# Kernel tuning notes

Hardware: AMD Instinct MI355X
Metric: run time of the kernel (lower is better)

## Reference

```python
import jax, jax.numpy as jnp
import numpy as np

N_HEADS = 16
HEAD_DIM = 64
D_MODEL = N_HEADS * HEAD_DIM  # 1024


def setup_inputs() -> dict:
    key = jax.random.key(0)
    ks = jax.random.split(key, 6)
    B, S, D = 2, 2048, D_MODEL
    s = 0.02
    return {
        "hidden_states": jax.random.normal(ks[0], (B, S, D), jnp.float32),
        "position_bias": jax.random.normal(ks[1], (1, N_HEADS, S, S), jnp.float32),
        "Wq": jax.random.normal(ks[2], (D, D), jnp.float32) * s,
        "Wk": jax.random.normal(ks[3], (D, D), jnp.float32) * s,
        "Wv": jax.random.normal(ks[4], (D, D), jnp.float32) * s,
        "Wo": jax.random.normal(ks[5], (D, D), jnp.float32) * s,
    }


def reference(hidden_states, position_bias, Wq, Wk, Wv, Wo):
    B, S, D = hidden_states.shape

    def split_heads(x):  # [B,S,D] -> [B,H,S,hd]
        return x.reshape(B, S, N_HEADS, HEAD_DIM).transpose(0, 2, 1, 3)

    q = split_heads(hidden_states @ Wq)
    k = split_heads(hidden_states @ Wk)
    v = split_heads(hidden_states @ Wv)

    # T5 attention: NO 1/sqrt(d) scaling; additive relative-position bias.
    scores = jnp.einsum("bhqd,bhkd->bhqk", q, k) + position_bias
    attn = jax.nn.softmax(scores.astype(jnp.float32), axis=-1).astype(scores.dtype)
    ctx = jnp.einsum("bhqk,bhkd->bhqd", attn, v)
    ctx = ctx.transpose(0, 2, 1, 3).reshape(B, S, D)
    return ctx @ Wo
```

## Files before the change

kernel.cpp:

```cpp
#include <hip/hip_runtime.h>
#include <hip/hip_bf16.h>
#include <stdint.h>

typedef __bf16 bf16_t;
typedef __bf16 bf16x8 __attribute__((ext_vector_type(8)));
typedef float  f32x4  __attribute__((ext_vector_type(4)));

#define S_LEN 2048
#define NH    16
#define HD    64
#define DM    1024
#define BATCH 2
#define M_TOT (BATCH * S_LEN)
#define SM_SHIFT 18.0f

__device__ __forceinline__ void gload16(const void* g, void* l) {
    __builtin_amdgcn_global_load_lds(
        (const __attribute__((address_space(1))) unsigned int*)g,
        (__attribute__((address_space(3))) unsigned int*)l, 16, 0, 0);
}

__global__ void convert_h(const float* __restrict__ X, bf16_t* __restrict__ Y, int n) {
    int i = (blockIdx.x * 256 + threadIdx.x) * 4;
    if (i >= n) return;
    float4 v = *(const float4*)(X + i);
    union { bf16_t h[4]; uint2 u; } pk;
    pk.h[0] = (bf16_t)v.x; pk.h[1] = (bf16_t)v.y;
    pk.h[2] = (bf16_t)v.z; pk.h[3] = (bf16_t)v.w;
    *(uint2*)(Y + i) = pk.u;
}

__global__ void convert_transpose_w(const float* __restrict__ W, bf16_t* __restrict__ Wt) {
    __shared__ float tile[32][33];
    const int tid = threadIdx.x;
    const int tx = tid & 31, ty = tid >> 5;
    const int bx = blockIdx.x * 32, by = blockIdx.y * 32;
#pragma unroll
    for (int it = 0; it < 4; ++it)
        tile[ty + it * 8][tx] = W[(size_t)(by + ty + it * 8) * DM + bx + tx];
    __syncthreads();
#pragma unroll
    for (int it = 0; it < 4; ++it)
        Wt[(size_t)(bx + ty + it * 8) * DM + by + tx] = (bf16_t)tile[tx][ty + it * 8];
}

template<int BN, int EPI>
__global__ __launch_bounds__(256)
void gemm_glds(const bf16_t* __restrict__ A, const bf16_t* __restrict__ Bt,
               float* __restrict__ Cf, bf16_t* __restrict__ Qb, bf16_t* __restrict__ Kb,
               bf16_t* __restrict__ Vtb, int M, int N, int K)
{
    constexpr int WN = BN / 2;
    constexpr int NJ = WN / 16;
    constexpr int RB = BN / 32;
    __shared__ bf16_t smem[16640];
    bf16_t* At  = smem;
    bf16_t* Bts = smem + 8192;

    const int tid  = threadIdx.x;
    const int lane = tid & 63;
    const int wave = tid >> 6;
    const int lc = lane & 15;
    const int l4 = lane >> 4;
    const int wr = wave >> 1, wc = wave & 1;
    const int m0 = blockIdx.y * 128;
    const int n0 = blockIdx.x * BN;
    const int srow = tid >> 3;
    const int scol = (tid & 7) * 8;

    f32x4 acc[4][NJ] = {};

    for (int k0 = 0; k0 < K; k0 += 64) {
        __syncthreads();
#pragma unroll
        for (int ro = 0; ro < 4; ++ro)
            gload16(A + (size_t)(m0 + ro * 32 + srow) * K + k0 + scol,
                    At + ro * 2048 + wave * 512);
#pragma unroll
        for (int ro = 0; ro < RB; ++ro)
            gload16(Bt + (size_t)(n0 + ro * 32 + srow) * K + k0 + scol,
                    Bts + ro * 2048 + wave * 512);
        __syncthreads();

        bf16x8 af[2][4], bfr[2][NJ];
#pragma unroll
        for (int kk = 0; kk < 2; ++kk) {
#pragma unroll
            for (int i = 0; i < 4; ++i)
                af[kk][i] = *(const bf16x8*)(At + (wr * 64 + i * 16 + lc) * 64 + kk * 32 + l4 * 8);
#pragma unroll
            for (int j = 0; j < NJ; ++j)
                bfr[kk][j] = *(const bf16x8*)(Bts + (wc * WN + j * 16 + lc) * 64 + kk * 32 + l4 * 8);
        }
#pragma unroll
        for (int kk = 0; kk < 2; ++kk)
#pragma unroll
            for (int i = 0; i < 4; ++i)
#pragma unroll
                for (int j = 0; j < NJ; ++j)
                    acc[i][j] = __builtin_amdgcn_mfma_f32_16x16x32_bf16(af[kk][i], bfr[kk][j], acc[i][j], 0, 0, 0);
    }

    if (EPI == 1) {
#pragma unroll
        for (int i = 0; i < 4; ++i)
#pragma unroll
            for (int j = 0; j < NJ; ++j)
#pragma unroll
                for (int r = 0; r < 4; ++r) {
                    int m = m0 + wr * 64 + i * 16 + l4 * 4 + r;
                    int n = n0 + wc * WN + j * 16 + lc;
                    Cf[(size_t)m * N + n] = acc[i][j][r];
                }
    } else {
        const int sel = n0 >> 10;
        if (sel < 2) {
            bf16_t* Dst = sel == 0 ? Qb : Kb;
#pragma unroll
            for (int i = 0; i < 4; ++i)
#pragma unroll
                for (int j = 0; j < NJ; ++j)
#pragma unroll
                    for (int r = 0; r < 4; ++r) {
                        int m = m0 + wr * 64 + i * 16 + l4 * 4 + r;
                        int n = (n0 & 1023) + wc * WN + j * 16 + lc;
                        int b = m >> 11, s = m & 2047, h = n >> 6, d = n & 63;
                        Dst[(((size_t)(b * NH + h)) * S_LEN + s) * HD + d] = (bf16_t)acc[i][j][r];
                    }
        } else {
            __syncthreads();
            bf16_t* Ct = smem;
#pragma unroll
            for (int i = 0; i < 4; ++i)
#pragma unroll
                for (int j = 0; j < NJ; ++j)
#pragma unroll
                    for (int r = 0; r < 4; ++r) {
                        int ml = wr * 64 + i * 16 + l4 * 4 + r;
                        int nl = wc * WN + j * 16 + lc;
                        Ct[nl * 130 + ml] = (bf16_t)acc[i][j][r];
                    }
            __syncthreads();
            const int rr = tid >> 1, c0 = (tid & 1) * 64;
            const int nn = (n0 - 2048) + rr;
            const int hh = nn >> 6, dd = nn & 63;
            const int bb = m0 >> 11, s0 = m0 & 2047;
            bf16_t* dst = Vtb + (((size_t)(bb * NH + hh)) * HD + dd) * S_LEN + s0 + c0;
            const bf16_t* srcr = Ct + rr * 130 + c0;
#pragma unroll
            for (int u = 0; u < 8; ++u)
                *(uint4*)(dst + u * 8) = *(const uint4*)(srcr + u * 8);
        }
    }
}

__global__ __launch_bounds__(256, 1)
void attn_kernel(const bf16_t* __restrict__ Q, const bf16_t* __restrict__ Kin,
                 const bf16_t* __restrict__ Vt, const float* __restrict__ bias,
                 bf16_t* __restrict__ Ctx)
{
    const int tid  = threadIdx.x;
    const int lane = tid & 63;
    const int wave = tid >> 6;
    const int lc = lane & 15;
    const int l4 = lane >> 4;

    const int f   = blockIdx.x;
    const int xcd = f & 7;
    const int kk_ = f >> 3;
    const int h   = xcd * 2 + (kk_ >> 4);
    const int qt  = kk_ & 15;
    const int qw  = qt * 128 + wave * 32;

    __shared__ bf16_t Kt[2][2][64 * 64];
    __shared__ bf16_t Vs[2][2][64 * 64];
    __shared__ bf16_t Pt[4][2][32 * 72];

    const bf16_t* Qg[2]; const bf16_t* Kg[2]; const bf16_t* Vg[2];
#pragma unroll
    for (int b = 0; b < 2; ++b) {
        const int bh = b * NH + h;
        Qg[b] = Q   + (size_t)bh * S_LEN * HD;
        Kg[b] = Kin + (size_t)bh * S_LEN * HD;
        Vg[b] = Vt  + (size_t)bh * HD * S_LEN;
    }
    const float* Bg = bias + (size_t)h * S_LEN * S_LEN;

    bf16x8 qf[2][2][2];
#pragma unroll
    for (int b = 0; b < 2; ++b)
#pragma unroll
        for (int i = 0; i < 2; ++i)
#pragma unroll
            for (int kk = 0; kk < 2; ++kk)
                qf[b][i][kk] = *(const bf16x8*)(Qg[b] + (size_t)(qw + i * 16 + lc) * HD + kk * 32 + l4 * 8);

    f32x4 cacc[2][2][4] = {};
    float lsum[2][2][4] = {};

    const int r0   = lane >> 3;
    const int gsrc = (lane & 7) ^ r0;

    auto stage = [&](int t, int pbuf) {
        const int kv0 = t * 64;
#pragma unroll
        for (int c = 0; c < 2; ++c) {
            const int row = c * 32 + wave * 8 + r0;
            const int ldsoff = (c * 32 + wave * 8) * 64;
#pragma unroll
            for (int b = 0; b < 2; ++b) {
                gload16(Kg[b] + (size_t)(kv0 + row) * HD + gsrc * 8, &Kt[b][pbuf][ldsoff]);
                gload16(Vg[b] + (size_t)row * S_LEN + kv0 + gsrc * 8, &Vs[b][pbuf][ldsoff]);
            }
        }
    };

    auto loadbias = [&](int t, float (&bv)[2][4][4]) {
        const int kv0 = t * 64;
#pragma unroll
        for (int i = 0; i < 2; ++i)
#pragma unroll
            for (int r = 0; r < 4; ++r) {
                const float* bp = Bg + (size_t)(qw + i * 16 + l4 * 4 + r) * S_LEN + kv0 + lc;
#pragma unroll
                for (int j = 0; j < 4; ++j)
                    bv[i][j][r] = bp[j * 16] - SM_SHIFT;
            }
    };

    auto round = [&](int t, float (&bcur)[2][4][4], float (&bnext)[2][4][4]) {
        const int buf = t & 1;
        if (t < 31) {
            stage(t + 1, buf ^ 1);
            loadbias(t + 1, bnext);
        }
#pragma unroll
        for (int b = 0; b < 2; ++b) {
            f32x4 sa[2][4] = {};
#pragma unroll
            for (int kk = 0; kk < 2; ++kk) {
                bf16x8 kf[4];
#pragma unroll
                for (int j = 0; j < 4; ++j)
                    kf[j] = *(const bf16x8*)(&Kt[b][buf][(j * 16 + lc) * 64 + (((kk * 4 + l4) ^ (lc & 7)) * 8)]);
#pragma unroll
                for (int i = 0; i < 2; ++i)
#pragma unroll
                    for (int j = 0; j < 4; ++j)
                        sa[i][j] = __builtin_amdgcn_mfma_f32_16x16x32_bf16(qf[b][i][kk], kf[j], sa[i][j], 0, 0, 0);
            }
            bf16_t* Pw = Pt[wave][b];
#pragma unroll
            for (int i = 0; i < 2; ++i)
#pragma unroll
                for (int r = 0; r < 4; ++r) {
                    float p0 = __expf(sa[i][0][r] + bcur[i][0][r]);
                    float p1 = __expf(sa[i][1][r] + bcur[i][1][r]);
                    float p2 = __expf(sa[i][2][r] + bcur[i][2][r]);
                    float p3 = __expf(sa[i][3][r] + bcur[i][3][r]);
                    lsum[b][i][r] += (p0 + p1) + (p2 + p3);
                    const int rowo = (i * 16 + l4 * 4 + r) * 72 + lc;
                    Pw[rowo]      = (bf16_t)p0;
                    Pw[rowo + 16] = (bf16_t)p1;
                    Pw[rowo + 32] = (bf16_t)p2;
                    Pw[rowo + 48] = (bf16_t)p3;
                }
#pragma unroll
            for (int ks = 0; ks < 2; ++ks) {
                bf16x8 pf[2], vf[4];
#pragma unroll
                for (int i = 0; i < 2; ++i)
                    pf[i] = *(const bf16x8*)(&Pw[(i * 16 + lc) * 72 + ks * 32 + l4 * 8]);
#pragma unroll
                for (int jd = 0; jd < 4; ++jd)
                    vf[jd] = *(const bf16x8*)(&Vs[b][buf][(jd * 16 + lc) * 64 + (((ks * 4 + l4) ^ (lc & 7)) * 8)]);
#pragma unroll
                for (int i = 0; i < 2; ++i)
#pragma unroll
                    for (int jd = 0; jd < 4; ++jd)
                        cacc[b][i][jd] = __builtin_amdgcn_mfma_f32_16x16x32_bf16(pf[i], vf[jd], cacc[b][i][jd], 0, 0, 0);
            }
        }
        __syncthreads();
    };

    float bvA[2][4][4], bvB[2][4][4];
    stage(0, 0);
    loadbias(0, bvA);
    __syncthreads();

    for (int ot = 0; ot < 16; ++ot) {
        round(2 * ot,     bvA, bvB);
        round(2 * ot + 1, bvB, bvA);
    }

#pragma unroll
    for (int d = 1; d < 16; d <<= 1)
#pragma unroll
        for (int b = 0; b < 2; ++b)
#pragma unroll
            for (int i = 0; i < 2; ++i)
#pragma unroll
                for (int r = 0; r < 4; ++r)
                    lsum[b][i][r] += __shfl_xor(lsum[b][i][r], d, 64);

#pragma unroll
    for (int b = 0; b < 2; ++b) {
        bf16_t* Co = Ctx + (size_t)b * S_LEN * DM + (size_t)h * HD;
#pragma unroll
        for (int i = 0; i < 2; ++i)
#pragma unroll
            for (int r = 0; r < 4; ++r) {
                float rinv = 1.0f / lsum[b][i][r];
                int qrow = qw + i * 16 + l4 * 4 + r;
#pragma unroll
                for (int jd = 0; jd < 4; ++jd)
                    Co[(size_t)qrow * DM + jd * 16 + lc] = (bf16_t)(cacc[b][i][jd][r] * rinv);
            }
    }
}

extern "C" void kernel_launch(void* const* d_in, const int* in_sizes, int n_in,
                              void* d_out, int out_size, void* d_ws, size_t ws_size,
                              hipStream_t stream)
{
    (void)in_sizes; (void)n_in; (void)out_size; (void)ws_size;
    const float* hs   = (const float*)d_in[0];
    const float* bias = (const float*)d_in[1];
    const float* Wq   = (const float*)d_in[2];
    const float* Wk   = (const float*)d_in[3];
    const float* Wv   = (const float*)d_in[4];
    const float* Wo   = (const float*)d_in[5];
    float* out = (float*)d_out;

    char* ws = (char*)d_ws;
    bf16_t* Hbf   = (bf16_t*)(ws);
    bf16_t* Wqkvt = (bf16_t*)(ws + ( 8u << 20));
    bf16_t* Wot   = (bf16_t*)(ws + (14u << 20));
    bf16_t* Qb    = (bf16_t*)(ws + (16u << 20));
    bf16_t* Kb    = (bf16_t*)(ws + (24u << 20));
    bf16_t* Vtb   = (bf16_t*)(ws + (32u << 20));
    bf16_t* Ctx   = (bf16_t*)(ws + (40u << 20));

    convert_h<<<4096, 256, 0, stream>>>(hs, Hbf, M_TOT * DM);
    dim3 tg(32, 32);
    convert_transpose_w<<<tg, 256, 0, stream>>>(Wq, Wqkvt);
    convert_transpose_w<<<tg, 256, 0, stream>>>(Wk, Wqkvt + (size_t)DM * DM);
    convert_transpose_w<<<tg, 256, 0, stream>>>(Wv, Wqkvt + (size_t)2 * DM * DM);
    convert_transpose_w<<<tg, 256, 0, stream>>>(Wo, Wot);

    dim3 gq(3 * DM / 128, M_TOT / 128);
    gemm_glds<128, 0><<<gq, 256, 0, stream>>>(Hbf, Wqkvt, nullptr, Qb, Kb, Vtb,
                                              M_TOT, 3 * DM, DM);

    attn_kernel<<<256, 256, 0, stream>>>(Qb, Kb, Vtb, bias, Ctx);

    dim3 go(DM / 64, M_TOT / 128);
    gemm_glds<64, 1><<<go, 256, 0, stream>>>(Ctx, Wot, out, nullptr, nullptr, nullptr,
                                             M_TOT, DM, DM);
}
```

Before: 215.6 us.

## Split attention batches across wave groups with 512-thread blocks and MFMA priority

The attention kernel now launches 512 threads per block. Waves 0-3 handle batch 0 and waves 4-7 handle batch 1, where previously each of 4 waves looped over both batches. This cuts per-wave register pressure (one batch of Q fragments and accumulators) and doubles the waves available to hide latency. The P scratch pitch shrinks from 72 to 68, and s_setprio is raised around the MFMA sections. Each bias value is still loaded per wave, so both batch groups now fetch the same bias separately and bias traffic may double.

After: 210.3 us. 1.03x faster.

```diff
diff --git a/kernel.cpp b/kernel.cpp
--- a/kernel.cpp
+++ b/kernel.cpp
@@ -154,7 +154,7 @@
     }
 }
 
-__global__ __launch_bounds__(256, 1)
+__global__ __launch_bounds__(512, 2)
 void attn_kernel(const bf16_t* __restrict__ Q, const bf16_t* __restrict__ Kin,
                  const bf16_t* __restrict__ Vt, const float* __restrict__ bias,
                  bf16_t* __restrict__ Ctx)
@@ -162,6 +162,8 @@
     const int tid  = threadIdx.x;
     const int lane = tid & 63;
     const int wave = tid >> 6;
+    const int b    = wave >> 2;
+    const int w    = wave & 3;
     const int lc = lane & 15;
     const int l4 = lane >> 4;
 
@@ -170,48 +172,44 @@
     const int kk_ = f >> 3;
     const int h   = xcd * 2 + (kk_ >> 4);
     const int qt  = kk_ & 15;
-    const int qw  = qt * 128 + wave * 32;
+    const int qw  = qt * 128 + w * 32;
 
     __shared__ bf16_t Kt[2][2][64 * 64];
     __shared__ bf16_t Vs[2][2][64 * 64];
-    __shared__ bf16_t Pt[4][2][32 * 72];
-
-    const bf16_t* Qg[2]; const bf16_t* Kg[2]; const bf16_t* Vg[2];
-#pragma unroll
-    for (int b = 0; b < 2; ++b) {
-        const int bh = b * NH + h;
-        Qg[b] = Q   + (size_t)bh * S_LEN * HD;
-        Kg[b] = Kin + (size_t)bh * S_LEN * HD;
-        Vg[b] = Vt  + (size_t)bh * HD * S_LEN;
+    __shared__ bf16_t Pt[8][32 * 68];
+
+    const int bh = b * NH + h;
+    const bf16_t* Qg = Q   + (size_t)bh * S_LEN * HD;
+    const bf16_t* Kg[2]; const bf16_t* Vg[2];
+#pragma unroll
+    for (int bb = 0; bb < 2; ++bb) {
+        Kg[bb] = Kin + (size_t)(bb * NH + h) * S_LEN * HD;
+        Vg[bb] = Vt  + (size_t)(bb * NH + h) * HD * S_LEN;
     }
     const float* Bg = bias + (size_t)h * S_LEN * S_LEN;
 
-    bf16x8 qf[2][2][2];
-#pragma unroll
-    for (int b = 0; b < 2; ++b)
-#pragma unroll
-        for (int i = 0; i < 2; ++i)
-#pragma unroll
-            for (int kk = 0; kk < 2; ++kk)
-                qf[b][i][kk] = *(const bf16x8*)(Qg[b] + (size_t)(qw + i * 16 + lc) * HD + kk * 32 + l4 * 8);
-
-    f32x4 cacc[2][2][4] = {};
-    float lsum[2][2][4] = {};
+    bf16x8 qf[2][2];
+#pragma unroll
+    for (int i = 0; i < 2; ++i)
+#pragma unroll
+        for (int kk = 0; kk < 2; ++kk)
+            qf[i][kk] = *(const bf16x8*)(Qg + (size_t)(qw + i * 16 + lc) * HD + kk * 32 + l4 * 8);
+
+    f32x4 cacc[2][4] = {};
+    float lsum[2][4] = {};
 
     const int r0   = lane >> 3;
     const int gsrc = (lane & 7) ^ r0;
+    const int sb   = wave >> 2;
+    const int z    = wave & 3;
 
     auto stage = [&](int t, int pbuf) {
         const int kv0 = t * 64;
 #pragma unroll
         for (int c = 0; c < 2; ++c) {
-            const int row = c * 32 + wave * 8 + r0;
-            const int ldsoff = (c * 32 + wave * 8) * 64;
-#pragma unroll
-            for (int b = 0; b < 2; ++b) {
-                gload16(Kg[b] + (size_t)(kv0 + row) * HD + gsrc * 8, &Kt[b][pbuf][ldsoff]);
-                gload16(Vg[b] + (size_t)row * S_LEN + kv0 + gsrc * 8, &Vs[b][pbuf][ldsoff]);
-            }
+            const int R = (c * 4 + z) * 8;
+            gload16(Kg[sb] + (size_t)(kv0 + R + r0) * HD + gsrc * 8, &Kt[sb][pbuf][R * 64]);
+            gload16(Vg[sb] + (size_t)(R + r0) * S_LEN + kv0 + gsrc * 8, &Vs[sb][pbuf][R * 64]);
         }
     };
 
@@ -227,6 +225,8 @@
                     bv[i][j][r] = bp[j * 16] - SM_SHIFT;
             }
     };
+
+    bf16_t* Pw = Pt[wave];
 
     auto round = [&](int t, float (&bcur)[2][4][4], float (&bnext)[2][4][4]) {
         const int buf = t & 1;
@@ -234,53 +234,53 @@
             stage(t + 1, buf ^ 1);
             loadbias(t + 1, bnext);
         }
-#pragma unroll
-        for (int b = 0; b < 2; ++b) {
-            f32x4 sa[2][4] = {};
-#pragma unroll
-            for (int kk = 0; kk < 2; ++kk) {
-                bf16x8 kf[4];
+        f32x4 sa[2][4] = {};
+        __builtin_amdgcn_s_setprio(1);
+#pragma unroll
+        for (int kk = 0; kk < 2; ++kk) {
+            bf16x8 kf[4];
+#pragma unroll
+            for (int j = 0; j < 4; ++j)
+                kf[j] = *(const bf16x8*)(&Kt[b][buf][(j * 16 + lc) * 64 + (((kk * 4 + l4) ^ (lc & 7)) * 8)]);
+#pragma unroll
+            for (int i = 0; i < 2; ++i)
 #pragma unroll
                 for (int j = 0; j < 4; ++j)
-                    kf[j] = *(const bf16x8*)(&Kt[b][buf][(j * 16 + lc) * 64 + (((kk * 4 + l4) ^ (lc & 7)) * 8)]);
-#pragma unroll
-                for (int i = 0; i < 2; ++i)
-#pragma unroll
-                    for (int j = 0; j < 4; ++j)
-                        sa[i][j] = __builtin_amdgcn_mfma_f32_16x16x32_bf16(qf[b][i][kk], kf[j], sa[i][j], 0, 0, 0);
+                    sa[i][j] = __builtin_amdgcn_mfma_f32_16x16x32_bf16(qf[i][kk], kf[j], sa[i][j], 0, 0, 0);
+        }
+        __builtin_amdgcn_s_setprio(0);
+#pragma unroll
+        for (int i = 0; i < 2; ++i)
+#pragma unroll
+            for (int r = 0; r < 4; ++r) {
+                float p0 = __expf(sa[i][0][r] + bcur[i][0][r]);
+                float p1 = __expf(sa[i][1][r] + bcur[i][1][r]);
+                float p2 = __expf(sa[i][2][r] + bcur[i][2][r]);
+                float p3 = __expf(sa[i][3][r] + bcur[i][3][r]);
+                lsum[i][r] += (p0 + p1) + (p2 + p3);
+                const int rowo = (i * 16 + l4 * 4 + r) * 68 + lc;
+                Pw[rowo]      = (bf16_t)p0;
+                Pw[rowo + 16] = (bf16_t)p1;
+                Pw[rowo + 32] = (bf16_t)p2;
+                Pw[rowo + 48] = (bf16_t)p3;
             }
-            bf16_t* Pw = Pt[wave][b];
+        __builtin_amdgcn_s_setprio(1);
+#pragma unroll
+        for (int ks = 0; ks < 2; ++ks) {
+            bf16x8 pf[2], vf[4];
 #pragma unroll
             for (int i = 0; i < 2; ++i)
-#pragma unroll
-                for (int r = 0; r < 4; ++r) {
-                    float p0 = __expf(sa[i][0][r] + bcur[i][0][r]);
-                    float p1 = __expf(sa[i][1][r] + bcur[i][1][r]);
-                    float p2 = __expf(sa[i][2][r] + bcur[i][2][r]);
-                    float p3 = __expf(sa[i][3][r] + bcur[i][3][r]);
-                    lsum[b][i][r] += (p0 + p1) + (p2 + p3);
-                    const int rowo = (i * 16 + l4 * 4 + r) * 72 + lc;
-                    Pw[rowo]      = (bf16_t)p0;
-                    Pw[rowo + 16] = (bf16_t)p1;
-                    Pw[rowo + 32] = (bf16_t)p2;
-                    Pw[rowo + 48] = (bf16_t)p3;
-                }
-#pragma unroll
-            for (int ks = 0; ks < 2; ++ks) {
-                bf16x8 pf[2], vf[4];
-#pragma unroll
-                for (int i = 0; i < 2; ++i)
-                    pf[i] = *(const bf16x8*)(&Pw[(i * 16 + lc) * 72 + ks * 32 + l4 * 8]);
+                pf[i] = *(const bf16x8*)(&Pw[(i * 16 + lc) * 68 + ks * 32 + l4 * 8]);
+#pragma unroll
+            for (int jd = 0; jd < 4; ++jd)
+                vf[jd] = *(const bf16x8*)(&Vs[b][buf][(jd * 16 + lc) * 64 + (((ks * 4 + l4) ^ (lc & 7)) * 8)]);
+#pragma unroll
+            for (int i = 0; i < 2; ++i)
 #pragma unroll
                 for (int jd = 0; jd < 4; ++jd)
-                    vf[jd] = *(const bf16x8*)(&Vs[b][buf][(jd * 16 + lc) * 64 + (((ks * 4 + l4) ^ (lc & 7)) * 8)]);
-#pragma unroll
-                for (int i = 0; i < 2; ++i)
-#pragma unroll
-                    for (int jd = 0; jd < 4; ++jd)
-                        cacc[b][i][jd] = __builtin_amdgcn_mfma_f32_16x16x32_bf16(pf[i], vf[jd], cacc[b][i][jd], 0, 0, 0);
-            }
-        }
+                    cacc[i][jd] = __builtin_amdgcn_mfma_f32_16x16x32_bf16(pf[i], vf[jd], cacc[i][jd], 0, 0, 0);
+        }
+        __builtin_amdgcn_s_setprio(0);
         __syncthreads();
     };
 
@@ -297,27 +297,22 @@
 #pragma unroll
     for (int d = 1; d < 16; d <<= 1)
 #pragma unroll
-        for (int b = 0; b < 2; ++b)
-#pragma unroll
-            for (int i = 0; i < 2; ++i)
-#pragma unroll
-                for (int r = 0; r < 4; ++r)
-                    lsum[b][i][r] += __shfl_xor(lsum[b][i][r], d, 64);
-
-#pragma unroll
-    for (int b = 0; b < 2; ++b) {
-        bf16_t* Co = Ctx + (size_t)b * S_LEN * DM + (size_t)h * HD;
-#pragma unroll
         for (int i = 0; i < 2; ++i)
 #pragma unroll
-            for (int r = 0; r < 4; ++r) {
-                float rinv = 1.0f / lsum[b][i][r];
-                int qrow = qw + i * 16 + l4 * 4 + r;
-#pragma unroll
-                for (int jd = 0; jd < 4; ++jd)
-                    Co[(size_t)qrow * DM + jd * 16 + lc] = (bf16_t)(cacc[b][i][jd][r] * rinv);
-            }
-    }
+            for (int r = 0; r < 4; ++r)
+                lsum[i][r] += __shfl_xor(lsum[i][r], d, 64);
+
+    bf16_t* Co = Ctx + (size_t)b * S_LEN * DM + (size_t)h * HD;
+#pragma unroll
+    for (int i = 0; i < 2; ++i)
+#pragma unroll
+        for (int r = 0; r < 4; ++r) {
+            float rinv = 1.0f / lsum[i][r];
+            int qrow = qw + i * 16 + l4 * 4 + r;
+#pragma unroll
+            for (int jd = 0; jd < 4; ++jd)
+                Co[(size_t)qrow * DM + jd * 16 + lc] = (bf16_t)(cacc[i][jd][r] * rinv);
+        }
 }
 
 extern "C" void kernel_launch(void* const* d_in, const int* in_sizes, int n_in,
@@ -353,7 +348,7 @@
     gemm_glds<128, 0><<<gq, 256, 0, stream>>>(Hbf, Wqkvt, nullptr, Qb, Kb, Vtb,
                                               M_TOT, 3 * DM, DM);
 
-    attn_kernel<<<256, 256, 0, stream>>>(Qb, Kb, Vtb, bias, Ctx);
+    attn_kernel<<<256, 512, 0, stream>>>(Qb, Kb, Vtb, bias, Ctx);
 
     dim3 go(DM / 64, M_TOT / 128);
     gemm_glds<64, 1><<<go, 256, 0, stream>>>(Ctx, Wot, out, nullptr, nullptr, nullptr,
```
